# Kernel optimization log

Hardware: AMD Instinct MI355X
Metric: run time of the kernel (lower is better)

Reference implementation:

```python
import jax, jax.numpy as jnp
import numpy as np

N_NODES = 100000


def setup_inputs() -> dict:
    key = jax.random.key(0)
    k1, k2, k3 = jax.random.split(key, 3)
    x = jax.random.normal(k1, (N_NODES, 128), dtype=jnp.float32)
    edge_index = jax.random.randint(k2, (2, 1600000), 0, N_NODES, dtype=jnp.int64)
    # TAGConv K=1 linear weight: maps concat([x, Ax]) (2*in) -> out; stored as [(K+1)*in, out]
    W = (jax.random.normal(k3, (256, 128), dtype=jnp.float32) / np.sqrt(256.0)).astype(jnp.float32)
    return {"x": x, "edge_index": edge_index, "W": W}


def reference(x, edge_index, W):
    src, dst = edge_index[0], edge_index[1]
    n = x.shape[0]
    ones = jnp.ones(src.shape[0], dtype=x.dtype)
    # gcn_norm without self-loops: degree from edge weights scattered at target
    deg = jax.ops.segment_sum(ones, dst, num_segments=n)
    dis = jnp.where(deg > 0, jax.lax.rsqrt(jnp.where(deg > 0, deg, 1.0)), 0.0)
    norm = dis[src] * dis[dst]  # [E]
    # message passing: out[dst] += norm * x[src]
    msgs = x[src] * norm[:, None]  # [E, in]
    agg = jax.ops.segment_sum(msgs, dst, num_segments=n)  # [N, in]
    h = jnp.concatenate([x, agg], axis=1)  # [N, 2*in]
    return h @ W  # [N, out]
```

## Files before the change

kernel.cpp:

```cpp
#include <hip/hip_runtime.h>


#define GCN_F 128
#define BINCAP 2560
#define EPACK_ROWS 15640

typedef __attribute__((ext_vector_type(8))) short frag_ab;
typedef __attribute__((ext_vector_type(4))) float frag_cd;

__device__ __forceinline__ unsigned short f2bf(float f) {
    unsigned int u = __float_as_uint(f);
    unsigned int r = (u + 0x7FFFu + ((u >> 16) & 1u)) >> 16;
    return (unsigned short)r;
}

__device__ __forceinline__ int detect_is32(const unsigned int* ei32, int* s_is32) {
    if (threadIdx.x == 0) *s_is32 = 0;
    __syncthreads();
    unsigned int v = 0;
    for (int i = threadIdx.x; i < 2048; i += blockDim.x) v |= ei32[2 * i + 1];
    if (v != 0u) atomicOr(s_is32, 1);
    __syncthreads();
    return *s_is32;
}

__device__ __forceinline__ int load_idx(const int* ei, int is32, long long pos) {
    if (is32) return ei[pos];
    return ((const int2*)ei)[pos].x;
}

__device__ __forceinline__ void xbf_store(const float4* x4, char* xb, int xs, int g) {
    int r = g >> 5, q = g & 31;
    float4 v = x4[(long long)r * 32 + q];
    ushort4 o;
    o.x = f2bf(v.x); o.y = f2bf(v.y); o.z = f2bf(v.z); o.w = f2bf(v.w);
    *(ushort4*)(xb + ((unsigned)r << xs) + q * 8) = o;
}

__global__ __launch_bounds__(256) void bscatter_kernel(const int* __restrict__ ei,
                                                       int* __restrict__ gcur,
                                                       unsigned int* __restrict__ epack,
                                                       int E, int EB, int nb,
                                                       const float* __restrict__ W,
                                                       unsigned short* __restrict__ wt,
                                                       const float4* __restrict__ x4,
                                                       char* __restrict__ xb,
                                                       int xs, int g0, int Ntot) {
    int tid = threadIdx.x;
    if ((int)blockIdx.x >= EB + 128) {
        int g = g0 + (blockIdx.x - (EB + 128)) * 256 + tid;
        if (g < Ntot * 32) xbf_store(x4, xb, xs, g);
        return;
    }
    if ((int)blockIdx.x >= EB) {
        int c = blockIdx.x - EB;
        wt[c * 256 + tid] = f2bf(W[tid * GCN_F + c]);
        return;
    }
    __shared__ int h[4][800];
    __shared__ int s_is32;
    int wv = tid >> 6;
    for (int i = tid; i < 4 * 800; i += 256) ((int*)h)[i] = 0;
    int is32 = detect_is32((const unsigned int*)ei, &s_is32);
    int base = blockIdx.x * 4096;
    unsigned int pk[16];
    int bn[16], rk[16];
#pragma unroll
    for (int j = 0; j < 16; ++j) bn[j] = -1;

#define BS_PROC(j, sv, dv_)                                          \
    {                                                                \
        unsigned int ud = (unsigned int)(dv_);                       \
        pk[j] = (unsigned int)(sv) | ((ud & 127u) << 17);            \
        int b_ = (int)(ud >> 7);                                     \
        bn[j] = b_;                                                  \
        rk[j] = atomicAdd(&h[wv][b_], 1);                            \
    }

    if (is32 && ((E & 3) == 0)) {
#pragma unroll
        for (int jj = 0; jj < 4; ++jj) {
            int e0 = base + jj * 1024 + tid * 4;
            if (e0 < E) {
                int4 s4 = *(const int4*)(ei + e0);
                int4 d4 = *(const int4*)(ei + (size_t)E + e0);
                int js = jj * 4;
                BS_PROC(js + 0, s4.x, d4.x); BS_PROC(js + 1, s4.y, d4.y);
                BS_PROC(js + 2, s4.z, d4.z); BS_PROC(js + 3, s4.w, d4.w);
            }
        }
    } else if (!is32) {
#pragma unroll
        for (int jj = 0; jj < 8; ++jj) {
            int e0 = base + jj * 512 + tid * 2;
            if (e0 + 1 < E) {
                int4 s2 = *(const int4*)((const int2*)ei + e0);
                int4 d2 = *(const int4*)((const int2*)ei + (size_t)E + e0);
                BS_PROC(jj * 2 + 0, s2.x, d2.x);
                BS_PROC(jj * 2 + 1, s2.z, d2.z);
            } else if (e0 < E) {
                int sv = ((const int2*)ei)[e0].x;
                int dv_ = ((const int2*)ei)[(size_t)E + e0].x;
                BS_PROC(jj * 2, sv, dv_);
            }
        }
    } else {
        for (int j = 0; j < 16; ++j) {
            int e = base + j * 256 + tid;
            if (e < E) {
                int sv = load_idx(ei, is32, e);
                int dv_ = load_idx(ei, is32, (long long)E + e);
                BS_PROC(j, sv, dv_);
            }
        }
    }
    __syncthreads();
    for (int b = tid; b < nb; b += 256) {
        int c0 = h[0][b], c1 = h[1][b], c2 = h[2][b], c3 = h[3][b];
        int tot = c0 + c1 + c2 + c3;
        int gbase = 0;
        if (tot > 0) {
            gbase = atomicAdd(&gcur[b], tot);
            if (gbase + tot > BINCAP) gbase = BINCAP - tot;
        }
        int p = b * BINCAP + gbase;
        h[0][b] = p;
        h[1][b] = p + c0;
        h[2][b] = p + c0 + c1;
        h[3][b] = p + c0 + c1 + c2;
    }
    __syncthreads();
#pragma unroll
    for (int j = 0; j < 16; ++j) {
        if (bn[j] >= 0) epack[h[wv][bn[j]] + rk[j]] = pk[j];
    }
#undef BS_PROC
}

__global__ __launch_bounds__(256) void fcsr_kernel(const unsigned int* __restrict__ epack,
                                                   const int* __restrict__ gcur,
                                                   int* __restrict__ start,
                                                   float* __restrict__ dis,
                                                   int* __restrict__ ebuf,
                                                   int N, int E) {
    __shared__ int red[256];
    __shared__ int lh[128];
    __shared__ int sc[128];
    int c = blockIdx.x;
    int tid = threadIdx.x;
    int partial = 0;
    for (int b = tid; b < c; b += 256) partial += min(gcur[b], BINCAP);
    red[tid] = partial;
    if (tid < 128) lh[tid] = 0;
    __syncthreads();
    for (int off = 128; off > 0; off >>= 1) {
        if (tid < off) red[tid] += red[tid + off];
        __syncthreads();
    }
    int s_base = red[0];
    int b0 = c * BINCAP;
    int e0 = b0 + min(gcur[c], BINCAP);
    for (int i = b0 + tid; i < e0; i += 256) {
        atomicAdd(&lh[(epack[i] >> 17) & 127u], 1);
    }
    __syncthreads();
    if (tid < 128) sc[tid] = lh[tid];
    __syncthreads();
    for (int off = 1; off < 128; off <<= 1) {
        int t = (tid < 128 && tid >= off) ? sc[tid - off] : 0;
        __syncthreads();
        if (tid < 128) sc[tid] += t;
        __syncthreads();
    }
    if (tid < 128) {
        int d = lh[tid];
        int gs = s_base + sc[tid] - d;
        int node = c * 128 + tid;
        if (node < N) {
            start[node] = gs;
            dis[node] = (d > 0) ? rsqrtf((float)d) : 0.0f;
        }
        sc[tid] = gs;
    }
    if (c == 0 && tid == 0) start[N] = E;
    __syncthreads();
    for (int i = b0 + tid; i < e0; i += 256) {
        unsigned int v = epack[i];
        int pos = atomicAdd(&sc[(v >> 17) & 127u], 1);
        ebuf[pos] = (int)(v & 0x1FFFFu);
    }
}

__global__ __launch_bounds__(256) void xbf_lo_kernel(const float4* __restrict__ x4,
                                                     char* __restrict__ xb, int xs) {
    int g = blockIdx.x * 256 + threadIdx.x;
    if (g >= EPACK_ROWS * 32) return;
    xbf_store(x4, xb, xs, g);
}

__global__ __launch_bounds__(256) void gather_kernel(const char* __restrict__ xb, int xs,
                                                     char* __restrict__ aggb,
                                                     const int* __restrict__ ebuf,
                                                     const int* __restrict__ start,
                                                     const float* __restrict__ dis,
                                                     int N) {
    int node = blockIdx.x * 4 + (threadIdx.x >> 6);
    if (node >= N) return;
    int lane = threadIdx.x & 63;
    int slot = lane >> 4;
    unsigned int subb = (lane & 15) * 16;
    int s = start[node];
    int d = start[node + 1] - s;
    float nd = dis[node];
    float acc[8];
#pragma unroll
    for (int i = 0; i < 8; ++i) acc[i] = 0.0f;

    for (int base = 0; base < d; base += 64) {
        int cn = min(64, d - base);
        int eid = 0; float dv = 0.0f;
        if (lane < cn) {
            eid = ebuf[s + base + lane];
            dv = dis[eid];
        }
        int njj = (cn + 3) >> 2;
#pragma unroll 4
        for (int j = 0; j < njj; ++j) {
            int tt = 4 * j + slot;
            int src = __shfl(eid, tt);
            float f = __shfl(dv, tt);
            uint4 u = *(const uint4*)(xb + (((unsigned)src << xs) + subb));
            acc[0] += f * __uint_as_float(u.x << 16);
            acc[1] += f * __uint_as_float(u.x);
            acc[2] += f * __uint_as_float(u.y << 16);
            acc[3] += f * __uint_as_float(u.y);
            acc[4] += f * __uint_as_float(u.z << 16);
            acc[5] += f * __uint_as_float(u.z);
            acc[6] += f * __uint_as_float(u.w << 16);
            acc[7] += f * __uint_as_float(u.w);
        }
    }
#pragma unroll
    for (int i = 0; i < 8; ++i) {
        acc[i] += __shfl_xor(acc[i], 16);
        acc[i] += __shfl_xor(acc[i], 32);
    }
    if (slot == 0) {
        uint4 o;
        o.x = (unsigned int)f2bf(acc[0] * nd) | ((unsigned int)f2bf(acc[1] * nd) << 16);
        o.y = (unsigned int)f2bf(acc[2] * nd) | ((unsigned int)f2bf(acc[3] * nd) << 16);
        o.z = (unsigned int)f2bf(acc[4] * nd) | ((unsigned int)f2bf(acc[5] * nd) << 16);
        o.w = (unsigned int)f2bf(acc[6] * nd) | ((unsigned int)f2bf(acc[7] * nd) << 16);
        *(uint4*)(aggb + (((unsigned)node << 9) + 256 + subb)) = o;
    }
}

#define GEMM_BM 128
__global__ __launch_bounds__(256) void gemm_mfma_kernel(
        const char* __restrict__ xb, int xs,
        const char* aggb,
        const unsigned short* __restrict__ wt,
        float* out, int N) {
    int wave = threadIdx.x >> 6;
    int lane = threadIdx.x & 63;
    int lr = lane & 15;
    int kh = lane >> 4;
    int rowbase = blockIdx.x * GEMM_BM + wave * 32;

    frag_cd acc[2][8];
#pragma unroll
    for (int rt = 0; rt < 2; ++rt)
#pragma unroll
        for (int ct = 0; ct < 8; ++ct) acc[rt][ct] = (frag_cd)0.0f;

#pragma unroll
    for (int ks = 0; ks < 8; ++ks) {
        frag_ab a[2];
#pragma unroll
        for (int rt = 0; rt < 2; ++rt) {
            int r = rowbase + rt * 16 + lr;
            r = min(r, N - 1);
            const char* ap = (ks < 4)
                ? (xb   + (((unsigned)r << xs) + (unsigned)(ks * 64 + kh * 16)))
                : (aggb + (((unsigned)r << 9) + (unsigned)(256 + (ks - 4) * 64 + kh * 16)));
            a[rt] = *(const frag_ab*)ap;
        }
#pragma unroll
        for (int ct = 0; ct < 8; ++ct) {
            int c = ct * 16 + lr;
            frag_ab b = *(const frag_ab*)(wt + c * 256 + ks * 32 + kh * 8);
#pragma unroll
            for (int rt = 0; rt < 2; ++rt) {
                acc[rt][ct] = __builtin_amdgcn_mfma_f32_16x16x32_bf16(a[rt], b, acc[rt][ct], 0, 0, 0);
            }
        }
    }
#pragma unroll
    for (int rt = 0; rt < 2; ++rt) {
#pragma unroll
        for (int ct = 0; ct < 8; ++ct) {
#pragma unroll
            for (int reg = 0; reg < 4; ++reg) {
                int r = rowbase + rt * 16 + kh * 4 + reg;
                if (r < N) out[r * GCN_F + ct * 16 + lr] = acc[rt][ct][reg];
            }
        }
    }
}

extern "C" void kernel_launch(void* const* d_in, const int* in_sizes, int n_in,
                              void* d_out, int out_size, void* d_ws, size_t ws_size,
                              hipStream_t stream) {
    const float* x  = (const float*)d_in[0];
    const int*   ei = (const int*)d_in[1];
    const float* W  = (const float*)d_in[2];
    float* out = (float*)d_out;

    const int N = in_sizes[0] / GCN_F;
    const int E = in_sizes[1] / 2;

    char* ws = (char*)d_ws;
    int*   gcur  = (int*)ws;
    float* dis   = (float*)(ws + 8192);
    int*   start = (int*)(ws + 408192);
    int*   ebuf  = (int*)(ws + 808208);
    unsigned short* wt = (unsigned short*)(ws + 7208208);
    char*  xb_ws = ws + 7274496;

    unsigned int* epack = (unsigned int*)d_out;
    char*         aggb  = (char*)d_out;

    const size_t WS_NEED = 7274496 + (size_t)N * 256;
    const bool bigws = ws_size >= WS_NEED;

    char* xb = bigws ? xb_ws : (char*)d_out;
    int   xs = bigws ? 8 : 9;
    int g0 = bigws ? 0 : EPACK_ROWS * 32;
    int XR = (N * 32 - g0 + 255) / 256;

    const int NB = (N + 127) / 128;
    const int EB = (E + 4095) / 4096;

    hipMemsetAsync(d_ws, 0, 4096, stream);

    bscatter_kernel<<<EB + 128 + XR, 256, 0, stream>>>(
        ei, gcur, epack, E, EB, NB, W, wt, (const float4*)x, xb, xs, g0, N);
    fcsr_kernel<<<NB, 256, 0, stream>>>(epack, gcur, start, dis, ebuf, N, E);
    if (!bigws) {
        xbf_lo_kernel<<<(EPACK_ROWS * 32 + 255) / 256, 256, 0, stream>>>(
            (const float4*)x, xb, xs);
    }
    gather_kernel<<<(N + 3) / 4, 256, 0, stream>>>(xb, xs, aggb, ebuf, start, dis, N);
    gemm_mfma_kernel<<<(N + GEMM_BM - 1) / GEMM_BM, 256, 0, stream>>>(
        xb, xs, aggb, wt, out, N);
}
```

Baseline: 158.8 us.

## Fuse all GCN stages into one cooperative persistent kernel with grid syncs

Replaces the memset plus four separate launches (bucket scatter, CSR build, gather, MFMA GEMM) with a single cooperative persistent kernel. Stages are separated by grid.sync and loop over work items with a grid-stride loop. The aim is to remove launch gaps and the host memset. The GEMM tile also shrinks from 128 to 64 rows per block. The trade-off is that grid size is capped at occupancy, so the gather and GEMM phases lose independent scheduling and pay grid-wide barrier costs.

```diff
diff --git a/kernel.cpp b/kernel.cpp
--- a/kernel.cpp
+++ b/kernel.cpp
@@ -1,4 +1,5 @@
 #include <hip/hip_runtime.h>
+#include <hip/hip_cooperative_groups.h>
 
 
 #define GCN_F 128
@@ -12,16 +13,6 @@
     unsigned int u = __float_as_uint(f);
     unsigned int r = (u + 0x7FFFu + ((u >> 16) & 1u)) >> 16;
     return (unsigned short)r;
-}
-
-__device__ __forceinline__ int detect_is32(const unsigned int* ei32, int* s_is32) {
-    if (threadIdx.x == 0) *s_is32 = 0;
-    __syncthreads();
-    unsigned int v = 0;
-    for (int i = threadIdx.x; i < 2048; i += blockDim.x) v |= ei32[2 * i + 1];
-    if (v != 0u) atomicOr(s_is32, 1);
-    __syncthreads();
-    return *s_is32;
 }
 
 __device__ __forceinline__ int load_idx(const int* ei, int is32, long long pos) {
@@ -35,6 +26,274 @@
     ushort4 o;
     o.x = f2bf(v.x); o.y = f2bf(v.y); o.z = f2bf(v.z); o.w = f2bf(v.w);
     *(ushort4*)(xb + ((unsigned)r << xs) + q * 8) = o;
+}
+
+__device__ __forceinline__ void gather_node(const char* xb, int xs, char* aggb,
+                                            const int* ebuf, const int* start,
+                                            const float* dis, int node, int tid) {
+    int lane = tid & 63;
+    int slot = lane >> 4;
+    unsigned int subb = (lane & 15) * 16;
+    int s = start[node];
+    int d = start[node + 1] - s;
+    float nd = dis[node];
+    float acc[8];
+#pragma unroll
+    for (int i = 0; i < 8; ++i) acc[i] = 0.0f;
+    for (int base = 0; base < d; base += 64) {
+        int cn = min(64, d - base);
+        int eid = 0; float dv = 0.0f;
+        if (lane < cn) {
+            eid = ebuf[s + base + lane];
+            dv = dis[eid];
+        }
+        int njj = (cn + 3) >> 2;
+#pragma unroll 4
+        for (int j = 0; j < njj; ++j) {
+            int tt = 4 * j + slot;
+            int src = __shfl(eid, tt);
+            float f = __shfl(dv, tt);
+            uint4 u = *(const uint4*)(xb + (((unsigned)src << xs) + subb));
+            acc[0] += f * __uint_as_float(u.x << 16);
+            acc[1] += f * __uint_as_float(u.x);
+            acc[2] += f * __uint_as_float(u.y << 16);
+            acc[3] += f * __uint_as_float(u.y);
+            acc[4] += f * __uint_as_float(u.z << 16);
+            acc[5] += f * __uint_as_float(u.z);
+            acc[6] += f * __uint_as_float(u.w << 16);
+            acc[7] += f * __uint_as_float(u.w);
+        }
+    }
+#pragma unroll
+    for (int i = 0; i < 8; ++i) {
+        acc[i] += __shfl_xor(acc[i], 16);
+        acc[i] += __shfl_xor(acc[i], 32);
+    }
+    if (slot == 0) {
+        uint4 o;
+        o.x = (unsigned int)f2bf(acc[0] * nd) | ((unsigned int)f2bf(acc[1] * nd) << 16);
+        o.y = (unsigned int)f2bf(acc[2] * nd) | ((unsigned int)f2bf(acc[3] * nd) << 16);
+        o.z = (unsigned int)f2bf(acc[4] * nd) | ((unsigned int)f2bf(acc[5] * nd) << 16);
+        o.w = (unsigned int)f2bf(acc[6] * nd) | ((unsigned int)f2bf(acc[7] * nd) << 16);
+        *(uint4*)(aggb + (((unsigned)node << 9) + 256 + subb)) = o;
+    }
+}
+
+struct MegaArgs {
+    const int* ei; int* gcur; unsigned int* epack;
+    int E, EB, NB, XR, N;
+    const float* W; unsigned short* wt;
+    const float4* x4; char* xb;
+    float* dis; int* start; int* ebuf;
+    char* aggb; float* out;
+};
+
+__global__ __launch_bounds__(256) void mega_kernel(MegaArgs A) {
+    namespace cg = cooperative_groups;
+    cg::grid_group grid = cg::this_grid();
+    __shared__ union SMU {
+        int h[3200];
+        struct { int red[256]; int lh[128]; int sc[128]; } f;
+    } sm;
+    __shared__ int s_is32;
+    const int tid = threadIdx.x;
+    const int bid = blockIdx.x;
+    const int gb = gridDim.x;
+
+    if (tid == 0) s_is32 = 0;
+    __syncthreads();
+    {
+        unsigned int v = 0;
+        const unsigned int* e32 = (const unsigned int*)A.ei;
+        for (int i = tid; i < 2048; i += 256) v |= e32[2 * i + 1];
+        if (v != 0u) atomicOr(&s_is32, 1);
+    }
+    __syncthreads();
+    const int is32 = s_is32;
+
+    for (int i = bid * 256 + tid; i < 1024; i += gb * 256) A.gcur[i] = 0;
+    for (int c = bid; c < 128; c += gb) A.wt[c * 256 + tid] = f2bf(A.W[tid * GCN_F + c]);
+    __threadfence();
+    grid.sync();
+
+    for (int w = bid; w < A.EB + A.XR; w += gb) {
+        if (w < A.EB) {
+            for (int i = tid; i < 3200; i += 256) sm.h[i] = 0;
+            __syncthreads();
+            int wv = tid >> 6;
+            int* hh = &sm.h[wv * 800];
+            int base = w * 4096;
+            unsigned int pk[16];
+            int bn[16], rk[16];
+#pragma unroll
+            for (int j = 0; j < 16; ++j) bn[j] = -1;
+#define BS_PROC(j, sv, dv_)                                       \
+    {                                                             \
+        unsigned int ud = (unsigned int)(dv_);                    \
+        pk[j] = (unsigned int)(sv) | ((ud & 127u) << 17);         \
+        int b_ = (int)(ud >> 7);                                  \
+        bn[j] = b_;                                               \
+        rk[j] = atomicAdd(&hh[b_], 1);                            \
+    }
+            if (is32 && ((A.E & 3) == 0)) {
+#pragma unroll
+                for (int jj = 0; jj < 4; ++jj) {
+                    int e0 = base + jj * 1024 + tid * 4;
+                    if (e0 < A.E) {
+                        int4 s4 = *(const int4*)(A.ei + e0);
+                        int4 d4 = *(const int4*)(A.ei + (size_t)A.E + e0);
+                        int js = jj * 4;
+                        BS_PROC(js + 0, s4.x, d4.x); BS_PROC(js + 1, s4.y, d4.y);
+                        BS_PROC(js + 2, s4.z, d4.z); BS_PROC(js + 3, s4.w, d4.w);
+                    }
+                }
+            } else if (!is32) {
+#pragma unroll
+                for (int jj = 0; jj < 8; ++jj) {
+                    int e0 = base + jj * 512 + tid * 2;
+                    if (e0 + 1 < A.E) {
+                        int4 s2 = *(const int4*)((const int2*)A.ei + e0);
+                        int4 d2 = *(const int4*)((const int2*)A.ei + (size_t)A.E + e0);
+                        BS_PROC(jj * 2 + 0, s2.x, d2.x);
+                        BS_PROC(jj * 2 + 1, s2.z, d2.z);
+                    } else if (e0 < A.E) {
+                        int sv = ((const int2*)A.ei)[e0].x;
+                        int dv_ = ((const int2*)A.ei)[(size_t)A.E + e0].x;
+                        BS_PROC(jj * 2, sv, dv_);
+                    }
+                }
+            } else {
+                for (int j = 0; j < 16; ++j) {
+                    int e = base + j * 256 + tid;
+                    if (e < A.E) {
+                        int sv = load_idx(A.ei, is32, e);
+                        int dv_ = load_idx(A.ei, is32, (long long)A.E + e);
+                        BS_PROC(j, sv, dv_);
+                    }
+                }
+            }
+#undef BS_PROC
+            __syncthreads();
+            for (int b = tid; b < A.NB; b += 256) {
+                int c0 = sm.h[b], c1 = sm.h[800 + b], c2 = sm.h[1600 + b], c3 = sm.h[2400 + b];
+                int tot = c0 + c1 + c2 + c3;
+                int gbase = 0;
+                if (tot > 0) {
+                    gbase = atomicAdd(&A.gcur[b], tot);
+                    if (gbase + tot > BINCAP) gbase = BINCAP - tot;
+                }
+                int p = b * BINCAP + gbase;
+                sm.h[b] = p;
+                sm.h[800 + b] = p + c0;
+                sm.h[1600 + b] = p + c0 + c1;
+                sm.h[2400 + b] = p + c0 + c1 + c2;
+            }
+            __syncthreads();
+#pragma unroll
+            for (int j = 0; j < 16; ++j) {
+                if (bn[j] >= 0) A.epack[hh[bn[j]] + rk[j]] = pk[j];
+            }
+            __syncthreads();
+        } else {
+            int g = (w - A.EB) * 256 + tid;
+            if (g < A.N * 32) xbf_store(A.x4, A.xb, 8, g);
+        }
+    }
+    __threadfence();
+    grid.sync();
+
+    for (int c = bid; c < A.NB; c += gb) {
+        int partial = 0;
+        for (int b = tid; b < c; b += 256) partial += min(A.gcur[b], BINCAP);
+        sm.f.red[tid] = partial;
+        if (tid < 128) sm.f.lh[tid] = 0;
+        __syncthreads();
+        for (int off = 128; off > 0; off >>= 1) {
+            if (tid < off) sm.f.red[tid] += sm.f.red[tid + off];
+            __syncthreads();
+        }
+        int s_base = sm.f.red[0];
+        int b0 = c * BINCAP;
+        int e0 = b0 + min(A.gcur[c], BINCAP);
+        for (int i = b0 + tid; i < e0; i += 256) {
+            atomicAdd(&sm.f.lh[(A.epack[i] >> 17) & 127u], 1);
+        }
+        __syncthreads();
+        if (tid < 128) sm.f.sc[tid] = sm.f.lh[tid];
+        __syncthreads();
+        for (int off = 1; off < 128; off <<= 1) {
+            int t = (tid < 128 && tid >= off) ? sm.f.sc[tid - off] : 0;
+            __syncthreads();
+            if (tid < 128) sm.f.sc[tid] += t;
+            __syncthreads();
+        }
+        if (tid < 128) {
+            int d = sm.f.lh[tid];
+            int gs = s_base + sm.f.sc[tid] - d;
+            int node = c * 128 + tid;
+            if (node < A.N) {
+                A.start[node] = gs;
+                A.dis[node] = (d > 0) ? rsqrtf((float)d) : 0.0f;
+            }
+            sm.f.sc[tid] = gs;
+        }
+        if (c == 0 && tid == 0) A.start[A.N] = A.E;
+        __syncthreads();
+        for (int i = b0 + tid; i < e0; i += 256) {
+            unsigned int v = A.epack[i];
+            int pos = atomicAdd(&sm.f.sc[(v >> 17) & 127u], 1);
+            A.ebuf[pos] = (int)(v & 0x1FFFFu);
+        }
+        __syncthreads();
+    }
+    __threadfence();
+    grid.sync();
+
+    {
+        int nq = (A.N + 3) >> 2;
+        for (int q = bid; q < nq; q += gb) {
+            int node = q * 4 + (tid >> 6);
+            if (node < A.N)
+                gather_node(A.xb, 8, A.aggb, A.ebuf, A.start, A.dis, node, tid);
+        }
+    }
+    __threadfence();
+    grid.sync();
+
+    {
+        int wave = tid >> 6;
+        int lane = tid & 63;
+        int lr = lane & 15;
+        int kh = lane >> 4;
+        int nt = (A.N + 63) >> 6;
+        for (int t = bid; t < nt; t += gb) {
+            int rowbase = t * 64 + wave * 16;
+            frag_cd acc[8];
+#pragma unroll
+            for (int ct = 0; ct < 8; ++ct) acc[ct] = (frag_cd)0.0f;
+#pragma unroll
+            for (int ks = 0; ks < 8; ++ks) {
+                int r = min(rowbase + lr, A.N - 1);
+                const char* ap = (ks < 4)
+                    ? (A.xb + (((unsigned)r << 8) + (unsigned)(ks * 64 + kh * 16)))
+                    : (A.aggb + (((unsigned)r << 9) + (unsigned)(256 + (ks - 4) * 64 + kh * 16)));
+                frag_ab a = *(const frag_ab*)ap;
+#pragma unroll
+                for (int ct = 0; ct < 8; ++ct) {
+                    frag_ab b = *(const frag_ab*)(A.wt + (ct * 16 + lr) * 256 + ks * 32 + kh * 8);
+                    acc[ct] = __builtin_amdgcn_mfma_f32_16x16x32_bf16(a, b, acc[ct], 0, 0, 0);
+                }
+            }
+#pragma unroll
+            for (int ct = 0; ct < 8; ++ct) {
+#pragma unroll
+                for (int reg = 0; reg < 4; ++reg) {
+                    int r = rowbase + kh * 4 + reg;
+                    if (r < A.N) A.out[r * GCN_F + ct * 16 + lr] = acc[ct][reg];
+                }
+            }
+        }
+    }
 }
 
 __global__ __launch_bounds__(256) void bscatter_kernel(const int* __restrict__ ei,
@@ -60,23 +319,30 @@
     __shared__ int h[4][800];
     __shared__ int s_is32;
     int wv = tid >> 6;
-    for (int i = tid; i < 4 * 800; i += 256) ((int*)h)[i] = 0;
-    int is32 = detect_is32((const unsigned int*)ei, &s_is32);
+    for (int i = tid; i < 3200; i += 256) ((int*)h)[i] = 0;
+    if (tid == 0) s_is32 = 0;
+    __syncthreads();
+    {
+        unsigned int v = 0;
+        const unsigned int* e32 = (const unsigned int*)ei;
+        for (int i = tid; i < 2048; i += 256) v |= e32[2 * i + 1];
+        if (v != 0u) atomicOr(&s_is32, 1);
+    }
+    __syncthreads();
+    int is32 = s_is32;
     int base = blockIdx.x * 4096;
     unsigned int pk[16];
     int bn[16], rk[16];
 #pragma unroll
     for (int j = 0; j < 16; ++j) bn[j] = -1;
-
-#define BS_PROC(j, sv, dv_)                                          \
-    {                                                                \
-        unsigned int ud = (unsigned int)(dv_);                       \
-        pk[j] = (unsigned int)(sv) | ((ud & 127u) << 17);            \
-        int b_ = (int)(ud >> 7);                                     \
-        bn[j] = b_;                                                  \
-        rk[j] = atomicAdd(&h[wv][b_], 1);                            \
-    }
-
+#define BS_PROC(j, sv, dv_)                                       \
+    {                                                             \
+        unsigned int ud = (unsigned int)(dv_);                    \
+        pk[j] = (unsigned int)(sv) | ((ud & 127u) << 17);         \
+        int b_ = (int)(ud >> 7);                                  \
+        bn[j] = b_;                                               \
+        rk[j] = atomicAdd(&h[wv][b_], 1);                         \
+    }
     if (is32 && ((E & 3) == 0)) {
 #pragma unroll
         for (int jj = 0; jj < 4; ++jj) {
@@ -114,6 +380,7 @@
             }
         }
     }
+#undef BS_PROC
     __syncthreads();
     for (int b = tid; b < nb; b += 256) {
         int c0 = h[0][b], c1 = h[1][b], c2 = h[2][b], c3 = h[3][b];
@@ -134,7 +401,6 @@
     for (int j = 0; j < 16; ++j) {
         if (bn[j] >= 0) epack[h[wv][bn[j]] + rk[j]] = pk[j];
     }
-#undef BS_PROC
 }
 
 __global__ __launch_bounds__(256) void fcsr_kernel(const unsigned int* __restrict__ epack,
@@ -206,53 +472,7 @@
                                                      int N) {
     int node = blockIdx.x * 4 + (threadIdx.x >> 6);
     if (node >= N) return;
-    int lane = threadIdx.x & 63;
-    int slot = lane >> 4;
-    unsigned int subb = (lane & 15) * 16;
-    int s = start[node];
-    int d = start[node + 1] - s;
-    float nd = dis[node];
-    float acc[8];
-#pragma unroll
-    for (int i = 0; i < 8; ++i) acc[i] = 0.0f;
-
-    for (int base = 0; base < d; base += 64) {
-        int cn = min(64, d - base);
-        int eid = 0; float dv = 0.0f;
-        if (lane < cn) {
-            eid = ebuf[s + base + lane];
-            dv = dis[eid];
-        }
-        int njj = (cn + 3) >> 2;
-#pragma unroll 4
-        for (int j = 0; j < njj; ++j) {
-            int tt = 4 * j + slot;
-            int src = __shfl(eid, tt);
-            float f = __shfl(dv, tt);
-            uint4 u = *(const uint4*)(xb + (((unsigned)src << xs) + subb));
-            acc[0] += f * __uint_as_float(u.x << 16);
-            acc[1] += f * __uint_as_float(u.x);
-            acc[2] += f * __uint_as_float(u.y << 16);
-            acc[3] += f * __uint_as_float(u.y);
-            acc[4] += f * __uint_as_float(u.z << 16);
-            acc[5] += f * __uint_as_float(u.z);
-            acc[6] += f * __uint_as_float(u.w << 16);
-            acc[7] += f * __uint_as_float(u.w);
-        }
-    }
-#pragma unroll
-    for (int i = 0; i < 8; ++i) {
-        acc[i] += __shfl_xor(acc[i], 16);
-        acc[i] += __shfl_xor(acc[i], 32);
-    }
-    if (slot == 0) {
-        uint4 o;
-        o.x = (unsigned int)f2bf(acc[0] * nd) | ((unsigned int)f2bf(acc[1] * nd) << 16);
-        o.y = (unsigned int)f2bf(acc[2] * nd) | ((unsigned int)f2bf(acc[3] * nd) << 16);
-        o.z = (unsigned int)f2bf(acc[4] * nd) | ((unsigned int)f2bf(acc[5] * nd) << 16);
-        o.w = (unsigned int)f2bf(acc[6] * nd) | ((unsigned int)f2bf(acc[7] * nd) << 16);
-        *(uint4*)(aggb + (((unsigned)node << 9) + 256 + subb)) = o;
-    }
+    gather_node(xb, xs, aggb, ebuf, start, dis, node, threadIdx.x);
 }
 
 #define GEMM_BM 128
@@ -266,13 +486,11 @@
     int lr = lane & 15;
     int kh = lane >> 4;
     int rowbase = blockIdx.x * GEMM_BM + wave * 32;
-
     frag_cd acc[2][8];
 #pragma unroll
     for (int rt = 0; rt < 2; ++rt)
 #pragma unroll
         for (int ct = 0; ct < 8; ++ct) acc[rt][ct] = (frag_cd)0.0f;
-
 #pragma unroll
     for (int ks = 0; ks < 8; ++ks) {
         frag_ab a[2];
@@ -281,14 +499,13 @@
             int r = rowbase + rt * 16 + lr;
             r = min(r, N - 1);
             const char* ap = (ks < 4)
-                ? (xb   + (((unsigned)r << xs) + (unsigned)(ks * 64 + kh * 16)))
+                ? (xb + (((unsigned)r << xs) + (unsigned)(ks * 64 + kh * 16)))
                 : (aggb + (((unsigned)r << 9) + (unsigned)(256 + (ks - 4) * 64 + kh * 16)));
             a[rt] = *(const frag_ab*)ap;
         }
 #pragma unroll
         for (int ct = 0; ct < 8; ++ct) {
-            int c = ct * 16 + lr;
-            frag_ab b = *(const frag_ab*)(wt + c * 256 + ks * 32 + kh * 8);
+            frag_ab b = *(const frag_ab*)(wt + (ct * 16 + lr) * 256 + ks * 32 + kh * 8);
 #pragma unroll
             for (int rt = 0; rt < 2; ++rt) {
                 acc[rt][ct] = __builtin_amdgcn_mfma_f32_16x16x32_bf16(a[rt], b, acc[rt][ct], 0, 0, 0);
@@ -333,16 +550,40 @@
     const size_t WS_NEED = 7274496 + (size_t)N * 256;
     const bool bigws = ws_size >= WS_NEED;
 
+    const int NB = (N + 127) / 128;
+    const int EB = (E + 4095) / 4096;
+    const int XR_ALL = (N * 32 + 255) / 256;
+
+    int coop = 0;
+    hipDeviceGetAttribute(&coop, hipDeviceAttributeCooperativeLaunch, 0);
+
+    int maxb = 0;
+    if (coop && bigws) {
+        hipOccupancyMaxActiveBlocksPerMultiprocessor(&maxb, mega_kernel, 256, 0);
+    }
+
+    if (coop && bigws && maxb > 0) {
+        hipDeviceProp_t prop;
+        hipGetDeviceProperties(&prop, 0);
+        int grid = maxb * prop.multiProcessorCount;
+        MegaArgs A;
+        A.ei = ei; A.gcur = gcur; A.epack = epack;
+        A.E = E; A.EB = EB; A.NB = NB; A.XR = XR_ALL; A.N = N;
+        A.W = W; A.wt = wt; A.x4 = (const float4*)x; A.xb = xb_ws;
+        A.dis = dis; A.start = start; A.ebuf = ebuf;
+        A.aggb = aggb; A.out = out;
+        void* kargs[] = {(void*)&A};
+        hipLaunchCooperativeKernel((void*)mega_kernel, dim3(grid), dim3(256),
+                                   kargs, 0, stream);
+        return;
+    }
+
     char* xb = bigws ? xb_ws : (char*)d_out;
     int   xs = bigws ? 8 : 9;
     int g0 = bigws ? 0 : EPACK_ROWS * 32;
     int XR = (N * 32 - g0 + 255) / 256;
 
-    const int NB = (N + 127) / 128;
-    const int EB = (E + 4095) / 4096;
-
     hipMemsetAsync(d_ws, 0, 4096, stream);
-
     bscatter_kernel<<<EB + 128 + XR, 256, 0, stream>>>(
         ei, gcur, epack, E, EB, NB, W, wt, (const float4*)x, xb, xs, g0, N);
     fcsr_kernel<<<NB, 256, 0, stream>>>(epack, gcur, start, dis, ebuf, N, E);
```

Measured after the change: 619.5 us. +290.0%, slower.

## Fuse neighbor gather and MFMA GEMM into one kernel via shared-memory aggregate tile

Applied to the files above, without the earlier changes.

When the workspace is large enough, a new fused kernel replaces the separate gather and GEMM kernels. Each block aggregates 64 nodes' neighbor features into a bf16 tile in shared memory, then runs the bf16 MFMA GEMM against W directly from that tile and from x. This removes the global write and re-read of the aggregate buffer and one kernel launch. In exchange the GEMM tile is smaller (64 rows, one 16-row tile per wave), and each block runs its gather and GEMM phases one after the other, which may lower occupancy or overlap. The rest is a refactor into shared helpers plus inlining the is32 detection.

```diff
diff --git a/kernel.cpp b/kernel.cpp
--- a/kernel.cpp
+++ b/kernel.cpp
@@ -12,16 +12,6 @@
     unsigned int u = __float_as_uint(f);
     unsigned int r = (u + 0x7FFFu + ((u >> 16) & 1u)) >> 16;
     return (unsigned short)r;
-}
-
-__device__ __forceinline__ int detect_is32(const unsigned int* ei32, int* s_is32) {
-    if (threadIdx.x == 0) *s_is32 = 0;
-    __syncthreads();
-    unsigned int v = 0;
-    for (int i = threadIdx.x; i < 2048; i += blockDim.x) v |= ei32[2 * i + 1];
-    if (v != 0u) atomicOr(s_is32, 1);
-    __syncthreads();
-    return *s_is32;
 }
 
 __device__ __forceinline__ int load_idx(const int* ei, int is32, long long pos) {
@@ -35,6 +25,54 @@
     ushort4 o;
     o.x = f2bf(v.x); o.y = f2bf(v.y); o.z = f2bf(v.z); o.w = f2bf(v.w);
     *(ushort4*)(xb + ((unsigned)r << xs) + q * 8) = o;
+}
+
+__device__ __forceinline__ void gather_acc(const char* xb, int xs,
+                                           const int* ebuf, const int* start,
+                                           const float* dis, int node, int lane,
+                                           int slot, unsigned int subb,
+                                           float* acc, float& nd) {
+    int s = start[node];
+    int d = start[node + 1] - s;
+    nd = dis[node];
+    for (int base = 0; base < d; base += 64) {
+        int cn = min(64, d - base);
+        int eid = 0; float dv = 0.0f;
+        if (lane < cn) {
+            eid = ebuf[s + base + lane];
+            dv = dis[eid];
+        }
+        int njj = (cn + 3) >> 2;
+#pragma unroll 4
+        for (int j = 0; j < njj; ++j) {
+            int tt = 4 * j + slot;
+            int src = __shfl(eid, tt);
+            float f = __shfl(dv, tt);
+            uint4 u = *(const uint4*)(xb + (((unsigned)src << xs) + subb));
+            acc[0] += f * __uint_as_float(u.x << 16);
+            acc[1] += f * __uint_as_float(u.x);
+            acc[2] += f * __uint_as_float(u.y << 16);
+            acc[3] += f * __uint_as_float(u.y);
+            acc[4] += f * __uint_as_float(u.z << 16);
+            acc[5] += f * __uint_as_float(u.z);
+            acc[6] += f * __uint_as_float(u.w << 16);
+            acc[7] += f * __uint_as_float(u.w);
+        }
+    }
+#pragma unroll
+    for (int i = 0; i < 8; ++i) {
+        acc[i] += __shfl_xor(acc[i], 16);
+        acc[i] += __shfl_xor(acc[i], 32);
+    }
+}
+
+__device__ __forceinline__ uint4 pack_bf8(const float* acc, float nd) {
+    uint4 o;
+    o.x = (unsigned int)f2bf(acc[0] * nd) | ((unsigned int)f2bf(acc[1] * nd) << 16);
+    o.y = (unsigned int)f2bf(acc[2] * nd) | ((unsigned int)f2bf(acc[3] * nd) << 16);
+    o.z = (unsigned int)f2bf(acc[4] * nd) | ((unsigned int)f2bf(acc[5] * nd) << 16);
+    o.w = (unsigned int)f2bf(acc[6] * nd) | ((unsigned int)f2bf(acc[7] * nd) << 16);
+    return o;
 }
 
 __global__ __launch_bounds__(256) void bscatter_kernel(const int* __restrict__ ei,
@@ -60,23 +98,30 @@
     __shared__ int h[4][800];
     __shared__ int s_is32;
     int wv = tid >> 6;
-    for (int i = tid; i < 4 * 800; i += 256) ((int*)h)[i] = 0;
-    int is32 = detect_is32((const unsigned int*)ei, &s_is32);
+    for (int i = tid; i < 3200; i += 256) ((int*)h)[i] = 0;
+    if (tid == 0) s_is32 = 0;
+    __syncthreads();
+    {
+        unsigned int v = 0;
+        const unsigned int* e32 = (const unsigned int*)ei;
+        for (int i = tid; i < 2048; i += 256) v |= e32[2 * i + 1];
+        if (v != 0u) atomicOr(&s_is32, 1);
+    }
+    __syncthreads();
+    int is32 = s_is32;
     int base = blockIdx.x * 4096;
     unsigned int pk[16];
     int bn[16], rk[16];
 #pragma unroll
     for (int j = 0; j < 16; ++j) bn[j] = -1;
-
-#define BS_PROC(j, sv, dv_)                                          \
-    {                                                                \
-        unsigned int ud = (unsigned int)(dv_);                       \
-        pk[j] = (unsigned int)(sv) | ((ud & 127u) << 17);            \
-        int b_ = (int)(ud >> 7);                                     \
-        bn[j] = b_;                                                  \
-        rk[j] = atomicAdd(&h[wv][b_], 1);                            \
-    }
-
+#define BS_PROC(j, sv, dv_)                                       \
+    {                                                             \
+        unsigned int ud = (unsigned int)(dv_);                    \
+        pk[j] = (unsigned int)(sv) | ((ud & 127u) << 17);         \
+        int b_ = (int)(ud >> 7);                                  \
+        bn[j] = b_;                                               \
+        rk[j] = atomicAdd(&h[wv][b_], 1);                         \
+    }
     if (is32 && ((E & 3) == 0)) {
 #pragma unroll
         for (int jj = 0; jj < 4; ++jj) {
@@ -114,6 +159,7 @@
             }
         }
     }
+#undef BS_PROC
     __syncthreads();
     for (int b = tid; b < nb; b += 256) {
         int c0 = h[0][b], c1 = h[1][b], c2 = h[2][b], c3 = h[3][b];
@@ -134,7 +180,6 @@
     for (int j = 0; j < 16; ++j) {
         if (bn[j] >= 0) epack[h[wv][bn[j]] + rk[j]] = pk[j];
     }
-#undef BS_PROC
 }
 
 __global__ __launch_bounds__(256) void fcsr_kernel(const unsigned int* __restrict__ epack,
@@ -191,6 +236,70 @@
     }
 }
 
+#define FBM 64
+__global__ __launch_bounds__(256) void gg_kernel(const char* __restrict__ xb,
+                                                 const int* __restrict__ ebuf,
+                                                 const int* __restrict__ start,
+                                                 const float* __restrict__ dis,
+                                                 const unsigned short* __restrict__ wt,
+                                                 float* __restrict__ out, int N) {
+    __shared__ unsigned short hagg[FBM][132];
+    int tid = threadIdx.x;
+    int wave = tid >> 6;
+    int lane = tid & 63;
+    int slot = lane >> 4;
+    unsigned int subb = (lane & 15) * 16;
+    int rowbase = blockIdx.x * FBM;
+
+    for (int q = 0; q < 16; ++q) {
+        int lr_ = q * 4 + wave;
+        int node = rowbase + lr_;
+        float acc[8];
+#pragma unroll
+        for (int i = 0; i < 8; ++i) acc[i] = 0.0f;
+        float nd = 0.0f;
+        if (node < N) {
+            gather_acc(xb, 8, ebuf, start, dis, node, lane, slot, subb, acc, nd);
+        }
+        if (slot == 0) {
+            uint4 o = pack_bf8(acc, nd);
+            *(uint4*)((char*)&hagg[lr_][0] + subb) = o;
+        }
+    }
+    __syncthreads();
+
+    int lr = lane & 15;
+    int kh = lane >> 4;
+    int rb = rowbase + wave * 16;
+    frag_cd acc2[8];
+#pragma unroll
+    for (int ct = 0; ct < 8; ++ct) acc2[ct] = (frag_cd)0.0f;
+#pragma unroll
+    for (int ks = 0; ks < 8; ++ks) {
+        frag_ab a;
+        if (ks < 4) {
+            int r = min(rb + lr, N - 1);
+            a = *(const frag_ab*)(xb + (((unsigned)r << 8) + (unsigned)(ks * 64 + kh * 16)));
+        } else {
+            int rloc = wave * 16 + lr;
+            a = *(const frag_ab*)((const char*)&hagg[rloc][0] + (ks - 4) * 64 + kh * 16);
+        }
+#pragma unroll
+        for (int ct = 0; ct < 8; ++ct) {
+            frag_ab b = *(const frag_ab*)(wt + (ct * 16 + lr) * 256 + ks * 32 + kh * 8);
+            acc2[ct] = __builtin_amdgcn_mfma_f32_16x16x32_bf16(a, b, acc2[ct], 0, 0, 0);
+        }
+    }
+#pragma unroll
+    for (int ct = 0; ct < 8; ++ct) {
+#pragma unroll
+        for (int reg = 0; reg < 4; ++reg) {
+            int r = rb + kh * 4 + reg;
+            if (r < N) out[r * GCN_F + ct * 16 + lr] = acc2[ct][reg];
+        }
+    }
+}
+
 __global__ __launch_bounds__(256) void xbf_lo_kernel(const float4* __restrict__ x4,
                                                      char* __restrict__ xb, int xs) {
     int g = blockIdx.x * 256 + threadIdx.x;
@@ -209,48 +318,13 @@
     int lane = threadIdx.x & 63;
     int slot = lane >> 4;
     unsigned int subb = (lane & 15) * 16;
-    int s = start[node];
-    int d = start[node + 1] - s;
-    float nd = dis[node];
     float acc[8];
 #pragma unroll
     for (int i = 0; i < 8; ++i) acc[i] = 0.0f;
-
-    for (int base = 0; base < d; base += 64) {
-        int cn = min(64, d - base);
-        int eid = 0; float dv = 0.0f;
-        if (lane < cn) {
-            eid = ebuf[s + base + lane];
-            dv = dis[eid];
-        }
-        int njj = (cn + 3) >> 2;
-#pragma unroll 4
-        for (int j = 0; j < njj; ++j) {
-            int tt = 4 * j + slot;
-            int src = __shfl(eid, tt);
-            float f = __shfl(dv, tt);
-            uint4 u = *(const uint4*)(xb + (((unsigned)src << xs) + subb));
-            acc[0] += f * __uint_as_float(u.x << 16);
-            acc[1] += f * __uint_as_float(u.x);
-            acc[2] += f * __uint_as_float(u.y << 16);
-            acc[3] += f * __uint_as_float(u.y);
-            acc[4] += f * __uint_as_float(u.z << 16);
-            acc[5] += f * __uint_as_float(u.z);
-            acc[6] += f * __uint_as_float(u.w << 16);
-            acc[7] += f * __uint_as_float(u.w);
-        }
-    }
-#pragma unroll
-    for (int i = 0; i < 8; ++i) {
-        acc[i] += __shfl_xor(acc[i], 16);
-        acc[i] += __shfl_xor(acc[i], 32);
-    }
+    float nd;
+    gather_acc(xb, xs, ebuf, start, dis, node, lane, slot, subb, acc, nd);
     if (slot == 0) {
-        uint4 o;
-        o.x = (unsigned int)f2bf(acc[0] * nd) | ((unsigned int)f2bf(acc[1] * nd) << 16);
-        o.y = (unsigned int)f2bf(acc[2] * nd) | ((unsigned int)f2bf(acc[3] * nd) << 16);
-        o.z = (unsigned int)f2bf(acc[4] * nd) | ((unsigned int)f2bf(acc[5] * nd) << 16);
-        o.w = (unsigned int)f2bf(acc[6] * nd) | ((unsigned int)f2bf(acc[7] * nd) << 16);
+        uint4 o = pack_bf8(acc, nd);
         *(uint4*)(aggb + (((unsigned)node << 9) + 256 + subb)) = o;
     }
 }
@@ -266,13 +340,11 @@
     int lr = lane & 15;
     int kh = lane >> 4;
     int rowbase = blockIdx.x * GEMM_BM + wave * 32;
-
     frag_cd acc[2][8];
 #pragma unroll
     for (int rt = 0; rt < 2; ++rt)
 #pragma unroll
         for (int ct = 0; ct < 8; ++ct) acc[rt][ct] = (frag_cd)0.0f;
-
 #pragma unroll
     for (int ks = 0; ks < 8; ++ks) {
         frag_ab a[2];
@@ -281,14 +353,13 @@
             int r = rowbase + rt * 16 + lr;
             r = min(r, N - 1);
             const char* ap = (ks < 4)
-                ? (xb   + (((unsigned)r << xs) + (unsigned)(ks * 64 + kh * 16)))
+                ? (xb + (((unsigned)r << xs) + (unsigned)(ks * 64 + kh * 16)))
                 : (aggb + (((unsigned)r << 9) + (unsigned)(256 + (ks - 4) * 64 + kh * 16)));
             a[rt] = *(const frag_ab*)ap;
         }
 #pragma unroll
         for (int ct = 0; ct < 8; ++ct) {
-            int c = ct * 16 + lr;
-            frag_ab b = *(const frag_ab*)(wt + c * 256 + ks * 32 + kh * 8);
+            frag_ab b = *(const frag_ab*)(wt + (ct * 16 + lr) * 256 + ks * 32 + kh * 8);
 #pragma unroll
             for (int rt = 0; rt < 2; ++rt) {
                 acc[rt][ct] = __builtin_amdgcn_mfma_f32_16x16x32_bf16(a[rt], b, acc[rt][ct], 0, 0, 0);
@@ -333,24 +404,27 @@
     const size_t WS_NEED = 7274496 + (size_t)N * 256;
     const bool bigws = ws_size >= WS_NEED;
 
+    const int NB = (N + 127) / 128;
+    const int EB = (E + 4095) / 4096;
+
     char* xb = bigws ? xb_ws : (char*)d_out;
     int   xs = bigws ? 8 : 9;
     int g0 = bigws ? 0 : EPACK_ROWS * 32;
     int XR = (N * 32 - g0 + 255) / 256;
 
-    const int NB = (N + 127) / 128;
-    const int EB = (E + 4095) / 4096;
-
     hipMemsetAsync(d_ws, 0, 4096, stream);
-
     bscatter_kernel<<<EB + 128 + XR, 256, 0, stream>>>(
         ei, gcur, epack, E, EB, NB, W, wt, (const float4*)x, xb, xs, g0, N);
     fcsr_kernel<<<NB, 256, 0, stream>>>(epack, gcur, start, dis, ebuf, N, E);
-    if (!bigws) {
+
+    if (bigws) {
+        gg_kernel<<<(N + FBM - 1) / FBM, 256, 0, stream>>>(
+            xb, ebuf, start, dis, wt, out, N);
+    } else {
         xbf_lo_kernel<<<(EPACK_ROWS * 32 + 255) / 256, 256, 0, stream>>>(
             (const float4*)x, xb, xs);
-    }
-    gather_kernel<<<(N + 3) / 4, 256, 0, stream>>>(xb, xs, aggb, ebuf, start, dis, N);
-    gemm_mfma_kernel<<<(N + GEMM_BM - 1) / GEMM_BM, 256, 0, stream>>>(
-        xb, xs, aggb, wt, out, N);
-}
+        gather_kernel<<<(N + 3) / 4, 256, 0, stream>>>(xb, xs, aggb, ebuf, start, dis, N);
+        gemm_mfma_kernel<<<(N + GEMM_BM - 1) / GEMM_BM, 256, 0, stream>>>(
+            xb, xs, aggb, wt, out, N);
+    }
+}
```

Result: slower. 206.5 us (+30.0%).
